# Kernel tuning notes

Hardware: AMD Instinct MI355X
Metric: run time of the kernel (lower is better)

The kernel has to match this reference:

```python
import jax, jax.numpy as jnp
import numpy as np

B, L, ENC_IN, C_OUT = 8, 8192, 21, 21
D_MODEL, D_STATE, D_CONV, EXPAND = 512, 16, 4, 2
D_INNER = EXPAND * D_MODEL
DT_RANK = -(-D_MODEL // 16)  # 'auto' -> ceil(d_model/16) = 32
PRED_LEN = 720


def setup_inputs() -> dict:
    key = jax.random.key(0)
    ks = jax.random.split(key, 16)
    s = lambda k, sh, sc=0.02: jax.random.normal(k, sh, jnp.float32) * sc
    # Mamba-style dt bias init: dt ~ exp(U(log dt_min, log dt_max)), bias = softplus^{-1}(dt)
    dt = jnp.exp(jax.random.uniform(ks[9], (D_INNER,), jnp.float32,
                                    float(np.log(1e-3)), float(np.log(0.1))))
    b_dt = jnp.log(jnp.expm1(dt))
    return dict(
        x_enc=jax.random.normal(ks[0], (B, L, ENC_IN), jnp.float32),
        x_mark_enc=jax.random.normal(ks[1], (B, L, 4), jnp.float32),
        x_dec=jax.random.normal(ks[2], (B, PRED_LEN, ENC_IN), jnp.float32),
        x_mark_dec=jax.random.normal(ks[3], (B, PRED_LEN, 4), jnp.float32),
        W_embed=s(ks[4], (ENC_IN, D_MODEL)),
        b_embed=jnp.zeros((D_MODEL,), jnp.float32),
        W_in=s(ks[5], (D_MODEL, 2 * D_INNER)),
        conv_w=s(ks[6], (D_INNER, D_CONV), 0.1),
        conv_b=jnp.zeros((D_INNER,), jnp.float32),
        W_xproj=s(ks[7], (D_INNER, DT_RANK + 2 * D_STATE)),
        W_dt=s(ks[8], (DT_RANK, D_INNER), 0.1),
        b_dt=b_dt,
        A_log=jnp.log(jnp.tile(jnp.arange(1, D_STATE + 1, dtype=jnp.float32), (D_INNER, 1))),
        D=jnp.ones((D_INNER,), jnp.float32),
        W_out_ssm=s(ks[10], (D_INNER, D_MODEL)),
        W_proj=s(ks[11], (D_MODEL, C_OUT)),
        b_proj=jnp.zeros((C_OUT,), jnp.float32),
    )


def _mamba(x, W_in, conv_w, conv_b, W_xproj, W_dt, b_dt, A_log, D):
    b, l, _ = x.shape
    d_inner, d_conv = conv_w.shape
    d_state = A_log.shape[1]
    dt_rank = W_dt.shape[0]
    xz = x @ W_in                                   # [b,l,2*d_inner]
    u, z = jnp.split(xz, 2, axis=-1)
    # causal depthwise conv over time
    uc = jnp.transpose(u, (0, 2, 1))                # [b,d_inner,l]
    uc = jax.lax.conv_general_dilated(uc, conv_w[:, None, :], (1,),
                                      [(d_conv - 1, 0)],
                                      feature_group_count=d_inner)
    u = jax.nn.silu(jnp.transpose(uc, (0, 2, 1)) + conv_b)
    x_dbl = u @ W_xproj
    dt, Bm, Cm = jnp.split(x_dbl, [dt_rank, dt_rank + d_state], axis=-1)
    delta = jax.nn.softplus(dt @ W_dt + b_dt)       # [b,l,d_inner]
    A = -jnp.exp(A_log)                             # [d_inner,d_state]

    def step(h, inp):
        d_t, B_t, C_t, u_t = inp                    # [b,d_inner],[b,d_state],[b,d_state],[b,d_inner]
        dA = jnp.exp(d_t[..., None] * A)            # [b,d_inner,d_state]
        h = dA * h + (d_t * u_t)[..., None] * B_t[:, None, :]
        y = jnp.einsum('bds,bs->bd', h, C_t)
        return h, y

    h0 = jnp.zeros((b, d_inner, d_state), u.dtype)
    xs = (jnp.moveaxis(delta, 1, 0), jnp.moveaxis(Bm, 1, 0),
          jnp.moveaxis(Cm, 1, 0), jnp.moveaxis(u, 1, 0))
    _, ys = jax.lax.scan(step, h0, xs)              # ys: [l,b,d_inner]
    y = jnp.moveaxis(ys, 0, 1) + u * D
    return y * jax.nn.silu(z)


def reference(x_enc, x_mark_enc, x_dec, x_mark_dec, W_embed, b_embed, W_in,
              conv_w, conv_b, W_xproj, W_dt, b_dt, A_log, D, W_out_ssm,
              W_proj, b_proj):
    # RevIN normalize (stats detached, matching .detach() in torch)
    means = jax.lax.stop_gradient(x_enc.mean(axis=1, keepdims=True))
    xc = x_enc - means
    stdev = jax.lax.stop_gradient(jnp.sqrt(jnp.var(xc, axis=1, keepdims=True) + 1e-5))
    xn = xc / stdev
    emb = xn @ W_embed + b_embed                    # [b,L,d_model]
    y = _mamba(emb, W_in, conv_w, conv_b, W_xproj, W_dt, b_dt, A_log, D)
    y = y @ W_out_ssm                               # [b,L,d_model]
    y = y[:, -PRED_LEN:, :]                         # L >= pred_len branch
    out = y @ W_proj + b_proj                       # [b,pred_len,c_out]
    out = out * stdev[:, :1, :] + means[:, :1, :]   # RevIN denorm (c_out == enc_in)
    return out
```

## Files before the change

### kernel.cpp

```cpp
#include <hip/hip_runtime.h>
#include <hip/hip_bf16.h>
#include <stdint.h>

#define B_    8
#define L_    8192
#define CIN   21
#define DM    512
#define DI    1024
#define DS    16
#define DTR   32
#define PRED  720
#define L0    (L_ - PRED)
#define CHUNK 128
#define NCHK  64
#define NTCH  6
#define TAIL0 7424
#define NSUB  24
#define TROWS 768

typedef __bf16 bf16_t;
typedef __attribute__((ext_vector_type(4))) __bf16 bf16x4;
typedef __attribute__((ext_vector_type(8))) __bf16 bf16x8;
typedef __attribute__((ext_vector_type(4))) float f32x4;

__device__ __forceinline__ void gl_lds16(const void* g, void* l) {
  __builtin_amdgcn_global_load_lds(
      (const __attribute__((address_space(1))) unsigned int*)g,
      (__attribute__((address_space(3))) unsigned int*)l, 16, 0, 0);
}

__device__ __forceinline__ float b2f(bf16_t v) { return (float)v; }
__device__ __forceinline__ bf16_t f2b(float v) { return (bf16_t)v; }

__device__ __forceinline__ void pow16(float r, float* pw) {
  float r2 = r * r, r4 = r2 * r2, r8 = r4 * r4, r3 = r2 * r;
  pw[0] = r;       pw[1] = r2;      pw[2] = r3;      pw[3] = r4;
  pw[4] = r4 * r;  pw[5] = r4 * r2; pw[6] = r4 * r3; pw[7] = r8;
  pw[8] = r8 * r;  pw[9] = r8 * r2; pw[10] = r8 * r3; pw[11] = r8 * r4;
  pw[12] = r8 * pw[4]; pw[13] = r8 * pw[5]; pw[14] = r8 * pw[6]; pw[15] = r8 * r8;
}

__global__ void zero_kernel(float* __restrict__ out, int n) {
  int i = blockIdx.x * 256 + threadIdx.x;
  if (i < n) out[i] = 0.f;
}

__global__ __launch_bounds__(256) void stats_kernel(const float* __restrict__ x,
                                                    float* __restrict__ stats) {
  const int b = blockIdx.x / CIN, c = blockIdx.x % CIN;
  const int tid = threadIdx.x;
  float s = 0.f, s2 = 0.f;
  for (int l = tid; l < L_; l += 256) {
    float v = x[((size_t)b * L_ + l) * CIN + c];
    s += v; s2 += v * v;
  }
  __shared__ float rs[256], rs2[256];
  rs[tid] = s; rs2[tid] = s2;
  __syncthreads();
  for (int o = 128; o > 0; o >>= 1) {
    if (tid < o) { rs[tid] += rs[tid + o]; rs2[tid] += rs2[tid + o]; }
    __syncthreads();
  }
  if (tid == 0) {
    float mean = rs[0] / (float)L_;
    float var  = rs2[0] / (float)L_ - mean * mean;
    stats[(b * CIN + c) * 2]     = mean;
    stats[(b * CIN + c) * 2 + 1] = sqrtf(var + 1e-5f);
  }
}

__global__ void tconv_kernel(const float* __restrict__ in, bf16_t* __restrict__ out,
                             int R, int C) {
  int idx = blockIdx.x * 256 + threadIdx.x;
  if (idx < R * C) {
    int r = idx / C, c = idx % C;
    out[(size_t)c * R + r] = f2b(in[idx]);
  }
}
__global__ void tconvf_kernel(const float* __restrict__ in, float* __restrict__ out,
                              int R, int C) {
  int idx = blockIdx.x * 256 + threadIdx.x;
  if (idx < R * C) {
    int r = idx / C, c = idx % C;
    out[(size_t)c * R + r] = in[idx];
  }
}

__global__ __launch_bounds__(256) void wcomb_kernel(const float* __restrict__ We,
                                                    const float* __restrict__ be,
                                                    const float* __restrict__ Win,
                                                    float* __restrict__ Wcu,
                                                    float* __restrict__ Wcz) {
  int idx = blockIdx.x * 256 + threadIdx.x;
  if (idx >= 22 * 2048) return;
  int c = idx / 2048, n = idx % 2048;
  float a = 0.f;
  if (c < 21) {
    for (int k = 0; k < DM; ++k) a = fmaf(We[c * DM + k], Win[(size_t)k * 2048 + n], a);
  } else {
    for (int k = 0; k < DM; ++k) a = fmaf(be[k], Win[(size_t)k * 2048 + n], a);
  }
  if (n < DI) Wcu[c * DI + n] = a;
  else        Wcz[c * DI + (n - DI)] = a;
}

__global__ __launch_bounds__(256) void fc_kernel(const float* __restrict__ x,
                                                 const float* __restrict__ stats,
                                                 const float* __restrict__ Wcu,
                                                 const float* __restrict__ cwT,
                                                 const float* __restrict__ cb,
                                                 bf16_t* __restrict__ u_act) {
  __shared__ float xn[11][22];
  const size_t bb = blockIdx.y;
  const float* xb = x + bb * ((size_t)L_ * CIN);
  const float* st = stats + bb * (CIN * 2);
  bf16_t* ua = u_act + bb * ((size_t)L_ * DI);
  const int r0 = blockIdx.x * 8;
  const int tid = threadIdx.x;
  for (int i = tid; i < 11 * 22; i += 256) {
    int j = i / 22, c = i % 22;
    int row = r0 - 3 + j;
    float v = 0.f;
    if (row >= 0) {
      if (c < 21) v = (xb[(size_t)row * CIN + c] - st[c * 2]) / st[c * 2 + 1];
      else v = 1.f;
    }
    xn[j][c] = v;
  }
  __syncthreads();
  const int col = tid * 4;
  f32x4 acc[11] = {};
  for (int c = 0; c < 22; ++c) {
    f32x4 w = *(const f32x4*)&Wcu[c * DI + col];
#pragma unroll
    for (int j = 0; j < 11; ++j) acc[j] += xn[j][c] * w;
  }
  f32x4 w0 = *(const f32x4*)&cwT[0 * DI + col];
  f32x4 w1 = *(const f32x4*)&cwT[1 * DI + col];
  f32x4 w2 = *(const f32x4*)&cwT[2 * DI + col];
  f32x4 w3 = *(const f32x4*)&cwT[3 * DI + col];
  f32x4 cbv = *(const f32x4*)&cb[col];
#pragma unroll
  for (int i = 0; i < 8; ++i) {
    f32x4 a = cbv + w0 * acc[i] + w1 * acc[i + 1] + w2 * acc[i + 2] + w3 * acc[i + 3];
    bf16x4 o;
#pragma unroll
    for (int e = 0; e < 4; ++e) {
      float v = a[e];
      o[e] = f2b(v / (1.f + __expf(-v)));
    }
    *(bf16x4*)&ua[(size_t)(r0 + i) * DI + col] = o;
  }
}

__global__ __launch_bounds__(256) void zfc_kernel(const float* __restrict__ x,
                                                  const float* __restrict__ stats,
                                                  const float* __restrict__ Wcz,
                                                  bf16_t* __restrict__ zbuf) {
  __shared__ float xn[22];
  const int row = blockIdx.x;
  const size_t b = blockIdx.y;
  const int tid = threadIdx.x;
  if (tid < 22) {
    int l = L0 + row;
    float v = 1.f;
    if (tid < 21)
      v = (x[(b * L_ + l) * (size_t)CIN + tid] - stats[(b * CIN + tid) * 2]) /
          stats[(b * CIN + tid) * 2 + 1];
    xn[tid] = v;
  }
  __syncthreads();
  const int col = tid * 4;
  f32x4 a = {};
  for (int c = 0; c < 22; ++c) a += xn[c] * *(const f32x4*)&Wcz[c * DI + col];
  bf16x4 o;
#pragma unroll
  for (int e = 0; e < 4; ++e) o[e] = f2b(a[e]);
  *(bf16x4*)&zbuf[(b * PRED + row) * (size_t)DI + col] = o;
}

template <int BM, int BN, int WMR, int WNR, int EPI>
__global__ __launch_bounds__(256) void gemm_kernel(
    const bf16_t* __restrict__ A, const bf16_t* __restrict__ Bt,
    bf16_t* __restrict__ O1, bf16_t* __restrict__ O1b, float* __restrict__ Of,
    int M, int N, int K, size_t sA, size_t sO1, size_t sO1b, size_t sOf) {
  __shared__ bf16_t Alds[BM][32];
  __shared__ bf16_t Blds[BN][32];
  const size_t zb = blockIdx.z;
  A += zb * sA;
  if (O1)  O1  += zb * sO1;
  if (O1b) O1b += zb * sO1b;
  if (Of)  Of  += zb * sOf;
  const int tid = threadIdx.x;
  const int wave = tid >> 6, lane = tid & 63;
  const int wm = wave >> 1, wn = wave & 1;
  const int lr = lane & 15, lk = lane >> 4;
  const int tm = blockIdx.x * BM;
  const int tn = blockIdx.y * BN;

  f32x4 acc[WMR][WNR] = {};

  const int nk = K >> 5;
  for (int ks = 0; ks < nk; ++ks) {
#pragma unroll
    for (int r = wave; r < BM / 16; r += 4)
      gl_lds16(A + (size_t)(tm + r * 16 + (lane >> 2)) * K + ks * 32 + (lane & 3) * 8,
               &Alds[r * 16][0]);
#pragma unroll
    for (int r = wave; r < BN / 16; r += 4)
      gl_lds16(Bt + (size_t)(tn + r * 16 + (lane >> 2)) * K + ks * 32 + (lane & 3) * 8,
               &Blds[r * 16][0]);
    __syncthreads();
    bf16x8 af[WMR], bfr[WNR];
#pragma unroll
    for (int mi = 0; mi < WMR; ++mi)
      af[mi] = *(const bf16x8*)(&Alds[wm * (WMR * 16) + mi * 16 + lr][lk * 8]);
#pragma unroll
    for (int ni = 0; ni < WNR; ++ni)
      bfr[ni] = *(const bf16x8*)(&Blds[wn * (WNR * 16) + ni * 16 + lr][lk * 8]);
#pragma unroll
    for (int mi = 0; mi < WMR; ++mi)
#pragma unroll
      for (int ni = 0; ni < WNR; ++ni)
        acc[mi][ni] = __builtin_amdgcn_mfma_f32_16x16x32_bf16(af[mi], bfr[ni], acc[mi][ni], 0, 0, 0);
    __syncthreads();
  }

#pragma unroll
  for (int mi = 0; mi < WMR; ++mi) {
#pragma unroll
    for (int ni = 0; ni < WNR; ++ni) {
#pragma unroll
      for (int r = 0; r < 4; ++r) {
        int row = tm + wm * (WMR * 16) + mi * 16 + lk * 4 + r;
        int col = tn + wn * (WNR * 16) + ni * 16 + lr;
        float v = acc[mi][ni][r];
        if constexpr (EPI == 0) {
          O1[(size_t)row * N + col] = f2b(v);
        } else if constexpr (EPI == 2) {
          if (col < 32) O1b[(size_t)row * 32 + col] = f2b(v);
          else          Of[(size_t)row * 32 + (col - 32)] = v;
        }
      }
    }
  }
}

__global__ __launch_bounds__(256) void scanA_kernel(
    const bf16_t* __restrict__ u_act, const bf16_t* __restrict__ dtb,
    const float* __restrict__ BC, const bf16_t* __restrict__ Wdt,
    const float* __restrict__ bdt,
    float* __restrict__ q, float* __restrict__ dsum_g,
    float* __restrict__ qs, float* __restrict__ dsums,
    bf16_t* __restrict__ dtail) {
  __shared__ __align__(16) char smem[53248];
  bf16_t (*Ul)[64] = (bf16_t(*)[64])smem;
  bf16_t (*Dl)[64] = (bf16_t(*)[64])(smem + 16384);
  bf16_t (*Dt)[32] = (bf16_t(*)[32])(smem + 32768);
  float  (*Bs)[16] = (float(*)[16])(smem + 40960);
  bf16_t (*Wl)[32] = (bf16_t(*)[32])(smem + 49152);
  const int tid = threadIdx.x, wave = tid >> 6, lane = tid & 63;
  const int d0 = blockIdx.x * 64, chunk = blockIdx.y;
  const size_t b = blockIdx.z;
  const bf16_t* ua = u_act + b * ((size_t)L_ * DI);
  const bf16_t* dt = dtb + b * ((size_t)L_ * 32);
  const float*  bc = BC + b * ((size_t)L_ * 32);
  const int row0 = chunk * CHUNK;
#pragma unroll
  for (int i = 0; i < 4; ++i)
    gl_lds16(ua + (size_t)(row0 + i * 32 + wave * 8 + (lane >> 3)) * DI + d0 + (lane & 7) * 8,
             &Ul[i * 32 + wave * 8][0]);
#pragma unroll
  for (int i = 0; i < 2; ++i)
    gl_lds16(dt + (size_t)(row0 + i * 64 + wave * 16 + (lane >> 2)) * 32 + (lane & 3) * 8,
             &Dt[i * 64 + wave * 16][0]);
#pragma unroll
  for (int i = 0; i < 2; ++i)
    gl_lds16(bc + (size_t)(row0 + i * 64 + wave * 16 + (lane >> 2)) * 32 + (lane & 3) * 4,
             &Bs[i * 64 + wave * 16][0]);
  gl_lds16(Wdt + (size_t)(d0 + wave * 16 + (lane >> 2)) * 32 + (lane & 3) * 8,
           &Wl[wave * 16][0]);
  __syncthreads();

  const int lr = lane & 15, lk = lane >> 4;
  const int m0 = wave * 32;
  bf16x8 af0 = *(const bf16x8*)&Dt[m0 + lr][lk * 8];
  bf16x8 af1 = *(const bf16x8*)&Dt[m0 + 16 + lr][lk * 8];
  f32x4 dacc[2][4];
#pragma unroll
  for (int ni = 0; ni < 4; ++ni) {
    bf16x8 bfr = *(const bf16x8*)&Wl[ni * 16 + lr][lk * 8];
    f32x4 zz = {};
    dacc[0][ni] = __builtin_amdgcn_mfma_f32_16x16x32_bf16(af0, bfr, zz, 0, 0, 0);
    dacc[1][ni] = __builtin_amdgcn_mfma_f32_16x16x32_bf16(af1, bfr, zz, 0, 0, 0);
  }
#pragma unroll
  for (int mi = 0; mi < 2; ++mi)
#pragma unroll
    for (int ni = 0; ni < 4; ++ni)
#pragma unroll
      for (int r = 0; r < 4; ++r) {
        int orow = m0 + mi * 16 + lk * 4 + r;
        int ocol = ni * 16 + lr;
        float xx = dacc[mi][ni][r] + bdt[d0 + ocol];
        float sp = (xx > 20.f) ? xx : log1pf(__expf(xx));
        Dl[orow][ocol] = f2b(sp);
      }
  __syncthreads();

  if (chunk >= NCHK - NTCH) {
    bf16_t* dtl = dtail + b * ((size_t)TROWS * DI) + (size_t)(row0 - TAIL0) * DI;
#pragma unroll
    for (int j = 0; j < 4; ++j) {
      int idx = j * 256 + tid;
      int rw = idx >> 3, cv = (idx & 7) * 8;
      *(bf16x8*)&dtl[(size_t)rw * DI + d0 + cv] = *(const bf16x8*)&Dl[rw][cv];
    }
  }

  float hs[16];
#pragma unroll
  for (int s = 0; s < 16; ++s) hs[s] = 0.f;
  float dsub = 0.f;
  const int t0 = wave * 32;
  for (int t = 0; t < 32; ++t) {
    float dlt = b2f(Dl[t0 + t][lane]);
    float ut  = b2f(Ul[t0 + t][lane]);
    float r = __expf(-dlt);
    float du = dlt * ut;
    dsub += dlt;
    float bv[16];
    *(f32x4*)&bv[0]  = *(const f32x4*)&Bs[t0 + t][0];
    *(f32x4*)&bv[4]  = *(const f32x4*)&Bs[t0 + t][4];
    *(f32x4*)&bv[8]  = *(const f32x4*)&Bs[t0 + t][8];
    *(f32x4*)&bv[12] = *(const f32x4*)&Bs[t0 + t][12];
    float pw[16];
    pow16(r, pw);
#pragma unroll
    for (int s = 0; s < 16; ++s)
      hs[s] = fmaf(pw[s], hs[s], du * bv[s]);
  }
  if (chunk >= NCHK - NTCH) {
    int si = (chunk - (NCHK - NTCH)) * 4 + wave;
    float* qs_b = qs + b * ((size_t)NSUB * 16 * DI);
    float* ds_b = dsums + b * ((size_t)NSUB * DI);
#pragma unroll
    for (int s = 0; s < 16; ++s)
      qs_b[((size_t)si * 16 + s) * DI + d0 + lane] = hs[s];
    ds_b[(size_t)si * DI + d0 + lane] = dsub;
  }
  __syncthreads();
  float (*Hw)[16][64] = (float(*)[16][64])(smem + 32768);
  float (*Dw)[64]     = (float(*)[64])(smem + 49152);
#pragma unroll
  for (int s = 0; s < 16; ++s) Hw[wave][s][lane] = hs[s];
  Dw[wave][lane] = dsub;
  __syncthreads();
  float* q_b = q + b * ((size_t)NCHK * 16 * DI);
  float* dg_b = dsum_g + b * ((size_t)NCHK * DI);
#pragma unroll
  for (int k = 0; k < 4; ++k) {
    const int d = tid & 63;
    const int s = (tid >> 6) + 4 * k;
    const float As = (float)(s + 1);
    float h = 0.f;
#pragma unroll
    for (int w = 0; w < 4; ++w)
      h = fmaf(__expf(-Dw[w][d] * As), h, Hw[w][s][d]);
    q_b[((size_t)chunk * 16 + s) * DI + d0 + d] = h;
  }
  if (tid < 64)
    dg_b[(size_t)chunk * DI + d0 + tid] = Dw[0][tid] + Dw[1][tid] + Dw[2][tid] + Dw[3][tid];
}

__global__ __launch_bounds__(256) void scanB_kernel(const float* __restrict__ q,
                                                    const float* __restrict__ dsum_g,
                                                    const float* __restrict__ qs,
                                                    const float* __restrict__ dsums,
                                                    float* __restrict__ h0) {
  const int idx = blockIdx.x * 256 + threadIdx.x;
  const int d = idx & (DI - 1);
  const int s = (idx >> 10) & 15;
  const size_t b = idx >> 14;
  const float As = (float)(s + 1);
  const float* q_b = q + b * ((size_t)NCHK * 16 * DI);
  const float* dg_b = dsum_g + b * ((size_t)NCHK * DI);
  const float* qs_b = qs + b * ((size_t)NSUB * 16 * DI);
  const float* ds_b = dsums + b * ((size_t)NSUB * DI);
  float* h0_b = h0 + b * ((size_t)NSUB * 16 * DI);
  float h = 0.f;
#pragma unroll 4
  for (int c = 0; c < NCHK - NTCH; ++c)
    h = fmaf(__expf(-dg_b[(size_t)c * DI + d] * As), h, q_b[((size_t)c * 16 + s) * DI + d]);
#pragma unroll 8
  for (int si = 0; si < NSUB; ++si) {
    h0_b[((size_t)si * 16 + s) * DI + d] = h;
    h = fmaf(__expf(-ds_b[(size_t)si * DI + d] * As), h, qs_b[((size_t)si * 16 + s) * DI + d]);
  }
}

__global__ __launch_bounds__(256) void scanC_kernel(
    const bf16_t* __restrict__ dl, const bf16_t* __restrict__ uu,
    const float* __restrict__ xt, const float* __restrict__ h0,
    const float* __restrict__ Dvec, const bf16_t* __restrict__ zb,
    bf16_t* __restrict__ yg, size_t sdl_b, size_t suu_b, size_t sxt_b) {
  __shared__ float Bs[32][16], Cs[32][16];
  const int tid = threadIdx.x;
  const int d = blockIdx.x * 256 + tid;
  const int sub = blockIdx.y + 1;
  const size_t b = blockIdx.z;
  const bf16_t* dlp = dl + b * sdl_b;
  const bf16_t* uup = uu + b * suu_b;
  const float*  xtp = xt + b * sxt_b;
  const bf16_t* zp  = zb + b * ((size_t)PRED * DI);
  bf16_t* yp = yg + b * ((size_t)PRED * DI);
  const int lr0 = sub * 32;
  for (int i = tid; i < 32 * 16; i += 256) {
    int t = i >> 4, s = i & 15;
    Bs[t][s] = xtp[(size_t)(lr0 + t) * 32 + s];
    Cs[t][s] = xtp[(size_t)(lr0 + t) * 32 + 16 + s];
  }
  __syncthreads();
  float h[16];
#pragma unroll
  for (int s = 0; s < 16; ++s)
    h[s] = h0[(b * NSUB + sub) * (size_t)(16 * DI) + (size_t)s * DI + d];
  const float Dd = Dvec[d];
#pragma unroll 8
  for (int t = 0; t < 32; ++t) {
    const int lr = lr0 + t;
    float dlt = b2f(dlp[(size_t)lr * DI + d]);
    float ut  = b2f(uup[(size_t)lr * DI + d]);
    float r = __expf(-dlt);
    float du = dlt * ut;
    float pw[16];
    pow16(r, pw);
    float y = 0.f;
#pragma unroll
    for (int s = 0; s < 16; ++s) {
      h[s] = fmaf(pw[s], h[s], du * Bs[t][s]);
      y = fmaf(h[s], Cs[t][s], y);
    }
    if (lr >= 48) {
      int gl = lr - 48;
      float zv = b2f(zp[(size_t)gl * DI + d]);
      float gate = zv / (1.f + __expf(-zv));
      yp[(size_t)gl * DI + d] = f2b((y + ut * Dd) * gate);
    }
  }
}

__global__ __launch_bounds__(256) void final_kernel(const bf16_t* __restrict__ y1,
                                                    const float* __restrict__ Wp,
                                                    const float* __restrict__ bp,
                                                    const float* __restrict__ stats,
                                                    float* __restrict__ out) {
  __shared__ float ys[DM];
  __shared__ float rs[8][32];
  const int row = blockIdx.x;
  const int b = row / PRED;
  const int tid = threadIdx.x;
  ys[tid] = b2f(y1[(size_t)row * DM + tid]);
  ys[tid + 256] = b2f(y1[(size_t)row * DM + tid + 256]);
  __syncthreads();
  const int c = tid & 31, ks = tid >> 5;
  float p = 0.f;
  if (c < CIN) {
    const int k0 = ks * 64;
    for (int k = 0; k < 64; ++k) p = fmaf(ys[k0 + k], Wp[(k0 + k) * CIN + c], p);
  }
  rs[ks][c] = p;
  __syncthreads();
  if (tid < CIN) {
    float a = bp[tid];
#pragma unroll
    for (int j = 0; j < 8; ++j) a += rs[j][tid];
    float mean = stats[(b * CIN + tid) * 2], sd = stats[(b * CIN + tid) * 2 + 1];
    out[(size_t)row * CIN + tid] = fmaf(a, sd, mean);
  }
}

static inline size_t padq(size_t x) { return (x + 255) & ~(size_t)255; }
struct Ptrs {
  bf16_t *u_act, *dtb, *dtail, *zbuf, *yg, *y1;
  bf16_t *Wt_xp, *Wt_dt, *Wt_out;
  float *BC, *q, *dsum, *qs, *dsums, *h0, *cwT, *Wcu, *Wcz, *stats;
  size_t total;
};
static Ptrs layout(char* ws) {
  Ptrs P; size_t off = 0;
  auto al = [&](size_t bytes) { char* p = ws + off; off += padq(bytes); return p; };
  P.u_act = (bf16_t*)al((size_t)B_ * L_ * DI * 2);
  P.dtb   = (bf16_t*)al((size_t)B_ * L_ * 32 * 2);
  P.BC    = (float*) al((size_t)B_ * L_ * 32 * 4);
  P.q     = (float*) al((size_t)B_ * NCHK * 16 * DI * 4);
  P.dsum  = (float*) al((size_t)B_ * NCHK * DI * 4);
  P.qs    = (float*) al((size_t)B_ * NSUB * 16 * DI * 4);
  P.dsums = (float*) al((size_t)B_ * NSUB * DI * 4);
  P.h0    = (float*) al((size_t)B_ * NSUB * 16 * DI * 4);
  P.dtail = (bf16_t*)al((size_t)B_ * TROWS * DI * 2);
  P.zbuf  = (bf16_t*)al((size_t)B_ * PRED * DI * 2);
  P.yg    = (bf16_t*)al((size_t)B_ * PRED * DI * 2);
  P.y1    = (bf16_t*)al((size_t)B_ * PRED * DM * 2);
  P.Wt_xp = (bf16_t*)al((size_t)64 * 1024 * 2);
  P.Wt_dt = (bf16_t*)al((size_t)1024 * 32 * 2);
  P.Wt_out= (bf16_t*)al((size_t)512 * 1024 * 2);
  P.cwT   = (float*) al((size_t)4 * DI * 4);
  P.Wcu   = (float*) al((size_t)22 * DI * 4);
  P.Wcz   = (float*) al((size_t)22 * DI * 4);
  P.stats = (float*) al((size_t)B_ * CIN * 2 * 4);
  P.total = off;
  return P;
}

extern "C" void kernel_launch(void* const* d_in, const int* in_sizes, int n_in,
                              void* d_out, int out_size, void* d_ws, size_t ws_size,
                              hipStream_t stream) {
  const float* x_enc   = (const float*)d_in[0];
  const float* W_embed = (const float*)d_in[4];
  const float* b_embed = (const float*)d_in[5];
  const float* W_in    = (const float*)d_in[6];
  const float* conv_w  = (const float*)d_in[7];
  const float* conv_b  = (const float*)d_in[8];
  const float* W_xproj = (const float*)d_in[9];
  const float* W_dt    = (const float*)d_in[10];
  const float* b_dt    = (const float*)d_in[11];
  const float* Dvec    = (const float*)d_in[13];
  const float* W_out   = (const float*)d_in[14];
  const float* W_proj  = (const float*)d_in[15];
  const float* b_proj  = (const float*)d_in[16];
  float* out = (float*)d_out;
  char* ws = (char*)d_ws;

  Ptrs P = layout(ws);
  if (P.total > ws_size) {
    zero_kernel<<<(out_size + 255) / 256, 256, 0, stream>>>(out, out_size);
    return;
  }

  stats_kernel<<<B_ * CIN, 256, 0, stream>>>(x_enc, P.stats);
  wcomb_kernel<<<(22 * 2048 + 255) / 256, 256, 0, stream>>>(W_embed, b_embed, W_in, P.Wcu, P.Wcz);
  tconv_kernel<<<(1024 * 64 + 255) / 256, 256, 0, stream>>>(W_xproj, P.Wt_xp, 1024, 64);
  tconv_kernel<<<(32 * 1024 + 255) / 256, 256, 0, stream>>>(W_dt,    P.Wt_dt, 32, 1024);
  tconv_kernel<<<(1024 * 512 + 255) / 256, 256, 0, stream>>>(W_out,   P.Wt_out, 1024, 512);
  tconvf_kernel<<<(1024 * 4 + 255) / 256, 256, 0, stream>>>(conv_w,  P.cwT, 1024, 4);

  zfc_kernel<<<dim3(PRED, B_), 256, 0, stream>>>(x_enc, P.stats, P.Wcz, P.zbuf);
  fc_kernel<<<dim3(L_ / 8, B_), 256, 0, stream>>>(x_enc, P.stats, P.Wcu, P.cwT, conv_b, P.u_act);
  gemm_kernel<32, 64, 1, 2, 2><<<dim3(L_ / 32, 1, B_), 256, 0, stream>>>(
      P.u_act, P.Wt_xp, nullptr, P.dtb, P.BC, L_, 64, DI,
      (size_t)L_ * DI, 0, (size_t)L_ * 32, (size_t)L_ * 32);
  scanA_kernel<<<dim3(DI / 64, NCHK, B_), 256, 0, stream>>>(
      P.u_act, P.dtb, P.BC, P.Wt_dt, b_dt, P.q, P.dsum, P.qs, P.dsums, P.dtail);
  scanB_kernel<<<(B_ * DI * DS) / 256, 256, 0, stream>>>(P.q, P.dsum, P.qs, P.dsums, P.h0);
  scanC_kernel<<<dim3(DI / 256, NSUB - 1, B_), 256, 0, stream>>>(
      P.dtail, P.u_act + (size_t)TAIL0 * DI, P.BC + (size_t)TAIL0 * 32, P.h0,
      Dvec, P.zbuf, P.yg,
      (size_t)TROWS * DI, (size_t)L_ * DI, (size_t)L_ * 32);
  gemm_kernel<64, 64, 2, 2, 0><<<dim3((B_ * PRED) / 64, DM / 64, 1), 256, 0, stream>>>(
      P.yg, P.Wt_out, P.y1, nullptr, nullptr, B_ * PRED, DM, DI, 0, 0, 0, 0);
  final_kernel<<<B_ * PRED, 256, 0, stream>>>(P.y1, W_proj, b_proj, P.stats, out);
}
```

Before: 522.4 us.

## Use packed f32x2 math and scalar B/C loads in scan kernels

Rewrites the chunked scan inner loops in scanA and scanC to keep state in f32x2 pairs so the compiler can emit packed FMA/multiply instructions, and computes the decay powers incrementally with paired multiplies. B and C rows are now read straight from global memory through a wave-uniform (readfirstlane) address, so they can become scalar loads, instead of being staged in LDS. scanA's shared memory is cut by overlaying buffers, and scanC skips the C dot product for rows that produce no output. The incremental power chain adds a serial dependency and may change rounding slightly.

```diff
diff --git a/kernel.cpp b/kernel.cpp
--- a/kernel.cpp
+++ b/kernel.cpp
@@ -22,6 +22,7 @@
 typedef __attribute__((ext_vector_type(4))) __bf16 bf16x4;
 typedef __attribute__((ext_vector_type(8))) __bf16 bf16x8;
 typedef __attribute__((ext_vector_type(4))) float f32x4;
+typedef __attribute__((ext_vector_type(2))) float f32x2;
 
 __device__ __forceinline__ void gl_lds16(const void* g, void* l) {
   __builtin_amdgcn_global_load_lds(
@@ -31,14 +32,6 @@
 
 __device__ __forceinline__ float b2f(bf16_t v) { return (float)v; }
 __device__ __forceinline__ bf16_t f2b(float v) { return (bf16_t)v; }
-
-__device__ __forceinline__ void pow16(float r, float* pw) {
-  float r2 = r * r, r4 = r2 * r2, r8 = r4 * r4, r3 = r2 * r;
-  pw[0] = r;       pw[1] = r2;      pw[2] = r3;      pw[3] = r4;
-  pw[4] = r4 * r;  pw[5] = r4 * r2; pw[6] = r4 * r3; pw[7] = r8;
-  pw[8] = r8 * r;  pw[9] = r8 * r2; pw[10] = r8 * r3; pw[11] = r8 * r4;
-  pw[12] = r8 * pw[4]; pw[13] = r8 * pw[5]; pw[14] = r8 * pw[6]; pw[15] = r8 * r8;
-}
 
 __global__ void zero_kernel(float* __restrict__ out, int n) {
   int i = blockIdx.x * 256 + threadIdx.x;
@@ -253,12 +246,11 @@
     float* __restrict__ q, float* __restrict__ dsum_g,
     float* __restrict__ qs, float* __restrict__ dsums,
     bf16_t* __restrict__ dtail) {
-  __shared__ __align__(16) char smem[53248];
+  __shared__ __align__(16) char smem[32768];
   bf16_t (*Ul)[64] = (bf16_t(*)[64])smem;
+  bf16_t (*Dt)[32] = (bf16_t(*)[32])(smem + 16384);
+  bf16_t (*Wl)[32] = (bf16_t(*)[32])(smem + 24576);
   bf16_t (*Dl)[64] = (bf16_t(*)[64])(smem + 16384);
-  bf16_t (*Dt)[32] = (bf16_t(*)[32])(smem + 32768);
-  float  (*Bs)[16] = (float(*)[16])(smem + 40960);
-  bf16_t (*Wl)[32] = (bf16_t(*)[32])(smem + 49152);
   const int tid = threadIdx.x, wave = tid >> 6, lane = tid & 63;
   const int d0 = blockIdx.x * 64, chunk = blockIdx.y;
   const size_t b = blockIdx.z;
@@ -274,10 +266,6 @@
   for (int i = 0; i < 2; ++i)
     gl_lds16(dt + (size_t)(row0 + i * 64 + wave * 16 + (lane >> 2)) * 32 + (lane & 3) * 8,
              &Dt[i * 64 + wave * 16][0]);
-#pragma unroll
-  for (int i = 0; i < 2; ++i)
-    gl_lds16(bc + (size_t)(row0 + i * 64 + wave * 16 + (lane >> 2)) * 32 + (lane & 3) * 4,
-             &Bs[i * 64 + wave * 16][0]);
   gl_lds16(Wdt + (size_t)(d0 + wave * 16 + (lane >> 2)) * 32 + (lane & 3) * 8,
            &Wl[wave * 16][0]);
   __syncthreads();
@@ -294,6 +282,7 @@
     dacc[0][ni] = __builtin_amdgcn_mfma_f32_16x16x32_bf16(af0, bfr, zz, 0, 0, 0);
     dacc[1][ni] = __builtin_amdgcn_mfma_f32_16x16x32_bf16(af1, bfr, zz, 0, 0, 0);
   }
+  __syncthreads();
 #pragma unroll
   for (int mi = 0; mi < 2; ++mi)
 #pragma unroll
@@ -318,42 +307,62 @@
     }
   }
 
-  float hs[16];
-#pragma unroll
-  for (int s = 0; s < 16; ++s) hs[s] = 0.f;
+  f32x2 h01{}, h23{}, h45{}, h67{}, h89{}, hab{}, hcd{}, hef{};
   float dsub = 0.f;
   const int t0 = wave * 32;
+#pragma unroll 4
   for (int t = 0; t < 32; ++t) {
+    int ridx = __builtin_amdgcn_readfirstlane(row0 + t0 + t);
+    const float* brow = bc + (size_t)ridx * 32;
+    f32x2 B0 = *(const f32x2*)(brow + 0);
+    f32x2 B1 = *(const f32x2*)(brow + 2);
+    f32x2 B2 = *(const f32x2*)(brow + 4);
+    f32x2 B3 = *(const f32x2*)(brow + 6);
+    f32x2 B4 = *(const f32x2*)(brow + 8);
+    f32x2 B5 = *(const f32x2*)(brow + 10);
+    f32x2 B6 = *(const f32x2*)(brow + 12);
+    f32x2 B7 = *(const f32x2*)(brow + 14);
     float dlt = b2f(Dl[t0 + t][lane]);
     float ut  = b2f(Ul[t0 + t][lane]);
-    float r = __expf(-dlt);
+    float rr = __expf(-dlt);
     float du = dlt * ut;
     dsub += dlt;
-    float bv[16];
-    *(f32x4*)&bv[0]  = *(const f32x4*)&Bs[t0 + t][0];
-    *(f32x4*)&bv[4]  = *(const f32x4*)&Bs[t0 + t][4];
-    *(f32x4*)&bv[8]  = *(const f32x4*)&Bs[t0 + t][8];
-    *(f32x4*)&bv[12] = *(const f32x4*)&Bs[t0 + t][12];
-    float pw[16];
-    pow16(r, pw);
-#pragma unroll
-    for (int s = 0; s < 16; ++s)
-      hs[s] = fmaf(pw[s], hs[s], du * bv[s]);
+    float r2s = rr * rr;
+    f32x2 p01 = {rr, r2s};
+    f32x2 rq  = {r2s, r2s};
+    f32x2 p23 = p01 * rq, p45 = p23 * rq, p67 = p45 * rq, p89 = p67 * rq,
+          pab = p89 * rq, pcd = pab * rq, pef = pcd * rq;
+    f32x2 du2 = {du, du};
+    h01 = p01 * h01 + du2 * B0;
+    h23 = p23 * h23 + du2 * B1;
+    h45 = p45 * h45 + du2 * B2;
+    h67 = p67 * h67 + du2 * B3;
+    h89 = p89 * h89 + du2 * B4;
+    hab = pab * hab + du2 * B5;
+    hcd = pcd * hcd + du2 * B6;
+    hef = pef * hef + du2 * B7;
   }
   if (chunk >= NCHK - NTCH) {
     int si = (chunk - (NCHK - NTCH)) * 4 + wave;
-    float* qs_b = qs + b * ((size_t)NSUB * 16 * DI);
+    float* qs_b = qs + b * ((size_t)NSUB * 16 * DI) + (size_t)si * 16 * DI + d0 + lane;
     float* ds_b = dsums + b * ((size_t)NSUB * DI);
-#pragma unroll
-    for (int s = 0; s < 16; ++s)
-      qs_b[((size_t)si * 16 + s) * DI + d0 + lane] = hs[s];
+    qs_b[0*DI]=h01[0];  qs_b[1*DI]=h01[1];  qs_b[2*DI]=h23[0];  qs_b[3*DI]=h23[1];
+    qs_b[4*DI]=h45[0];  qs_b[5*DI]=h45[1];  qs_b[6*DI]=h67[0];  qs_b[7*DI]=h67[1];
+    qs_b[8*DI]=h89[0];  qs_b[9*DI]=h89[1];  qs_b[10*DI]=hab[0]; qs_b[11*DI]=hab[1];
+    qs_b[12*DI]=hcd[0]; qs_b[13*DI]=hcd[1]; qs_b[14*DI]=hef[0]; qs_b[15*DI]=hef[1];
     ds_b[(size_t)si * DI + d0 + lane] = dsub;
   }
   __syncthreads();
-  float (*Hw)[16][64] = (float(*)[16][64])(smem + 32768);
-  float (*Dw)[64]     = (float(*)[64])(smem + 49152);
-#pragma unroll
-  for (int s = 0; s < 16; ++s) Hw[wave][s][lane] = hs[s];
+  float (*Hw)[16][64] = (float(*)[16][64])smem;
+  float (*Dw)[64]     = (float(*)[64])(smem + 16384);
+  Hw[wave][0][lane]=h01[0];  Hw[wave][1][lane]=h01[1];
+  Hw[wave][2][lane]=h23[0];  Hw[wave][3][lane]=h23[1];
+  Hw[wave][4][lane]=h45[0];  Hw[wave][5][lane]=h45[1];
+  Hw[wave][6][lane]=h67[0];  Hw[wave][7][lane]=h67[1];
+  Hw[wave][8][lane]=h89[0];  Hw[wave][9][lane]=h89[1];
+  Hw[wave][10][lane]=hab[0]; Hw[wave][11][lane]=hab[1];
+  Hw[wave][12][lane]=hcd[0]; Hw[wave][13][lane]=hcd[1];
+  Hw[wave][14][lane]=hef[0]; Hw[wave][15][lane]=hef[1];
   Dw[wave][lane] = dsub;
   __syncthreads();
   float* q_b = q + b * ((size_t)NCHK * 16 * DI);
@@ -401,10 +410,9 @@
 
 __global__ __launch_bounds__(256) void scanC_kernel(
     const bf16_t* __restrict__ dl, const bf16_t* __restrict__ uu,
-    const float* __restrict__ xt, const float* __restrict__ h0,
+    const float* __restrict__ xt, const float* __restrict__ h0buf,
     const float* __restrict__ Dvec, const bf16_t* __restrict__ zb,
     bf16_t* __restrict__ yg, size_t sdl_b, size_t suu_b, size_t sxt_b) {
-  __shared__ float Bs[32][16], Cs[32][16];
   const int tid = threadIdx.x;
   const int d = blockIdx.x * 256 + tid;
   const int sub = blockIdx.y + 1;
@@ -415,33 +423,57 @@
   const bf16_t* zp  = zb + b * ((size_t)PRED * DI);
   bf16_t* yp = yg + b * ((size_t)PRED * DI);
   const int lr0 = sub * 32;
-  for (int i = tid; i < 32 * 16; i += 256) {
-    int t = i >> 4, s = i & 15;
-    Bs[t][s] = xtp[(size_t)(lr0 + t) * 32 + s];
-    Cs[t][s] = xtp[(size_t)(lr0 + t) * 32 + 16 + s];
-  }
-  __syncthreads();
-  float h[16];
-#pragma unroll
-  for (int s = 0; s < 16; ++s)
-    h[s] = h0[(b * NSUB + sub) * (size_t)(16 * DI) + (size_t)s * DI + d];
+  const float* hp = h0buf + (b * NSUB + sub) * (size_t)(16 * DI) + d;
+  f32x2 h01 = {hp[0*DI], hp[1*DI]},   h23 = {hp[2*DI], hp[3*DI]},
+        h45 = {hp[4*DI], hp[5*DI]},   h67 = {hp[6*DI], hp[7*DI]},
+        h89 = {hp[8*DI], hp[9*DI]},   hab = {hp[10*DI], hp[11*DI]},
+        hcd = {hp[12*DI], hp[13*DI]}, hef = {hp[14*DI], hp[15*DI]};
   const float Dd = Dvec[d];
-#pragma unroll 8
+#pragma unroll 4
   for (int t = 0; t < 32; ++t) {
     const int lr = lr0 + t;
+    int ridx = __builtin_amdgcn_readfirstlane(lr);
+    const float* brow = xtp + (size_t)ridx * 32;
+    f32x2 B0 = *(const f32x2*)(brow + 0);
+    f32x2 B1 = *(const f32x2*)(brow + 2);
+    f32x2 B2 = *(const f32x2*)(brow + 4);
+    f32x2 B3 = *(const f32x2*)(brow + 6);
+    f32x2 B4 = *(const f32x2*)(brow + 8);
+    f32x2 B5 = *(const f32x2*)(brow + 10);
+    f32x2 B6 = *(const f32x2*)(brow + 12);
+    f32x2 B7 = *(const f32x2*)(brow + 14);
     float dlt = b2f(dlp[(size_t)lr * DI + d]);
     float ut  = b2f(uup[(size_t)lr * DI + d]);
-    float r = __expf(-dlt);
+    float rr = __expf(-dlt);
     float du = dlt * ut;
-    float pw[16];
-    pow16(r, pw);
-    float y = 0.f;
-#pragma unroll
-    for (int s = 0; s < 16; ++s) {
-      h[s] = fmaf(pw[s], h[s], du * Bs[t][s]);
-      y = fmaf(h[s], Cs[t][s], y);
-    }
+    float r2s = rr * rr;
+    f32x2 p01 = {rr, r2s};
+    f32x2 rq  = {r2s, r2s};
+    f32x2 p23 = p01 * rq, p45 = p23 * rq, p67 = p45 * rq, p89 = p67 * rq,
+          pab = p89 * rq, pcd = pab * rq, pef = pcd * rq;
+    f32x2 du2 = {du, du};
+    h01 = p01 * h01 + du2 * B0;
+    h23 = p23 * h23 + du2 * B1;
+    h45 = p45 * h45 + du2 * B2;
+    h67 = p67 * h67 + du2 * B3;
+    h89 = p89 * h89 + du2 * B4;
+    hab = pab * hab + du2 * B5;
+    hcd = pcd * hcd + du2 * B6;
+    hef = pef * hef + du2 * B7;
     if (lr >= 48) {
+      f32x2 C0 = *(const f32x2*)(brow + 16);
+      f32x2 C1 = *(const f32x2*)(brow + 18);
+      f32x2 C2 = *(const f32x2*)(brow + 20);
+      f32x2 C3 = *(const f32x2*)(brow + 22);
+      f32x2 C4 = *(const f32x2*)(brow + 24);
+      f32x2 C5 = *(const f32x2*)(brow + 26);
+      f32x2 C6 = *(const f32x2*)(brow + 28);
+      f32x2 C7 = *(const f32x2*)(brow + 30);
+      f32x2 ya = h01 * C0;
+      ya = h23 * C1 + ya; ya = h45 * C2 + ya; ya = h67 * C3 + ya;
+      ya = h89 * C4 + ya; ya = hab * C5 + ya; ya = hcd * C6 + ya;
+      ya = hef * C7 + ya;
+      float y = ya[0] + ya[1];
       int gl = lr - 48;
       float zv = b2f(zp[(size_t)gl * DI + d]);
       float gate = zv / (1.f + __expf(-zv));
```

New measurement: 515.0 us. No clear change (-1.4%).
